# Optimization experiments

Measured on AMD Instinct MI355X. Metric: run time of the kernel, lower is better.

## Reference

```python
import jax, jax.numpy as jnp
import numpy as np

NPTS = 16
IN_FEATURES = 3


def setup_inputs() -> dict:
    key = jax.random.key(0)
    x = jax.random.uniform(key, (8, IN_FEATURES, 512, 512), dtype=jnp.float32)
    # parameters, matching the torch module's initialization
    shifts = np.linspace(0, 1, NPTS, endpoint=False, dtype=np.float32)[:, None]
    shift = jnp.asarray(np.tile(shifts, (1, IN_FEATURES)))          # (npts, C)
    slopes = np.zeros((NPTS, IN_FEATURES), dtype=np.float32)
    slopes[0, :] = 1.0
    slopes = jnp.asarray(slopes)                                    # (npts, C)
    conv_w = jnp.full((IN_FEATURES,), 1.0 / IN_FEATURES, dtype=jnp.float32)  # 1x1 conv C->1
    conv_b = jnp.zeros((1,), dtype=jnp.float32)
    return {"x": x, "shift": shift, "slopes": slopes, "conv_w": conv_w, "conv_b": conv_b}


def reference(x, shift, slopes, conv_w, conv_b):
    # x: (B, C, H, W); shift/slopes: (npts, C)
    # piecewise-linear curve: sum_p slopes[p,c] * relu(x - shift[p,c])
    curves = slopes[None, :, :, None, None] * jax.nn.relu(
        x[:, None, :, :, :] - shift[None, :, :, None, None]
    )                                   # (B, npts, C, H, W)
    y = jnp.sum(curves, axis=1)         # (B, C, H, W)
    # 1x1 conv C -> 1 with bias, then hardtanh(0, 1)
    out = jnp.einsum("bchw,c->bhw", y, conv_w)[:, None, :, :] + conv_b[None, :, None, None]
    return jnp.clip(out, 0.0, 1.0)      # (B, 1, H, W)
```

## Files before the change

kernel.cpp:

```cpp
#include <hip/hip_runtime.h>
#include <hip/hip_bf16.h>


constexpr int NPTS = 16;
constexpr int C    = 3;
constexpr int HW   = 512 * 512;
constexpr int HW4  = HW / 4;

__global__ __launch_bounds__(256)
void curve_channel_kernel(const float4* __restrict__ x,
                          const float*  __restrict__ shift,
                          const float*  __restrict__ slopes,
                          const float*  __restrict__ conv_w,
                          const float*  __restrict__ conv_b,
                          float4*       __restrict__ out,
                          int n4)
{
    const int idx = blockIdx.x * 256 + threadIdx.x;
    if (idx >= n4) return;

    const int b   = idx >> 16;
    const int hw4 = idx & (HW4 - 1);

    const float4* xb = x + (size_t)b * (C * HW4) + hw4;

    const float bias = conv_b[0];
    float ax = bias, ay = bias, az = bias, aw = bias;

#pragma unroll
    for (int c = 0; c < C; ++c) {
        const float4 xv = xb[(size_t)c * HW4];
        const float  w  = conv_w[c];
        float yx = 0.f, yy = 0.f, yz = 0.f, yw = 0.f;
#pragma unroll
        for (int p = 0; p < NPTS; ++p) {
            const float s = shift[p * C + c];
            const float m = slopes[p * C + c];
            yx += m * fmaxf(xv.x - s, 0.f);
            yy += m * fmaxf(xv.y - s, 0.f);
            yz += m * fmaxf(xv.z - s, 0.f);
            yw += m * fmaxf(xv.w - s, 0.f);
        }
        ax += w * yx;
        ay += w * yy;
        az += w * yz;
        aw += w * yw;
    }

    float4 o;
    o.x = fminf(fmaxf(ax, 0.f), 1.f);
    o.y = fminf(fmaxf(ay, 0.f), 1.f);
    o.z = fminf(fmaxf(az, 0.f), 1.f);
    o.w = fminf(fmaxf(aw, 0.f), 1.f);
    out[idx] = o;
}

extern "C" void kernel_launch(void* const* d_in, const int* in_sizes, int n_in,
                              void* d_out, int out_size, void* d_ws, size_t ws_size,
                              hipStream_t stream)
{
    const float* x      = (const float*)d_in[0];
    const float* shift  = (const float*)d_in[1];
    const float* slopes = (const float*)d_in[2];
    const float* conv_w = (const float*)d_in[3];
    const float* conv_b = (const float*)d_in[4];
    float*       out    = (float*)d_out;

    const int n4     = out_size / 4;
    const int blocks = (n4 + 255) / 256;

    curve_channel_kernel<<<dim3(blocks), dim3(256), 0, stream>>>(
        (const float4*)x, shift, slopes, conv_w, conv_b, (float4*)out, n4);
}
```

Measured before the change: 82.10 us.

## Rewrite relu sum via abs identity, process two float4 per thread, nontemporal stores

Uses relu(x-s) = 0.5*((x-s)+|x-s|) to fold the linear part into per-channel constants A and B, so each breakpoint costs one sub, one abs-modifier and one FMA instead of a max, a multiply and an add. Each thread now handles two float4 groups, which halves the grid and amortizes the shift/slope parameter loads. Output is written with nontemporal stores. The kernel is largely memory bound (about 25 MB read, 8 MB written), so the ALU savings may matter little, and the extra registers could reduce occupancy.

```diff
diff --git a/kernel.cpp b/kernel.cpp
--- a/kernel.cpp
+++ b/kernel.cpp
@@ -1,58 +1,78 @@
 #include <hip/hip_runtime.h>
-#include <hip/hip_bf16.h>
 
+
+typedef float f4v __attribute__((ext_vector_type(4)));
 
 constexpr int NPTS = 16;
 constexpr int C    = 3;
-constexpr int HW   = 512 * 512;
-constexpr int HW4  = HW / 4;
+constexpr int HW4  = 65536;
 
 __global__ __launch_bounds__(256)
-void curve_channel_kernel(const float4* __restrict__ x,
-                          const float*  __restrict__ shift,
-                          const float*  __restrict__ slopes,
-                          const float*  __restrict__ conv_w,
-                          const float*  __restrict__ conv_b,
-                          float4*       __restrict__ out,
+void curve_channel_kernel(const f4v*  __restrict__ x,
+                          const float* __restrict__ shift,
+                          const float* __restrict__ slopes,
+                          const float* __restrict__ conv_w,
+                          const float* __restrict__ conv_b,
+                          f4v*        __restrict__ out,
                           int n4)
 {
-    const int idx = blockIdx.x * 256 + threadIdx.x;
-    if (idx >= n4) return;
+    const int i0 = blockIdx.x * 512 + (int)threadIdx.x;
+    if (i0 >= n4) return;
+    const int  i1   = i0 + 256;
+    const bool has1 = (i1 < n4);
 
-    const int b   = idx >> 16;
-    const int hw4 = idx & (HW4 - 1);
-
-    const float4* xb = x + (size_t)b * (C * HW4) + hw4;
+    const int b0 = i0 >> 16, h0 = i0 & (HW4 - 1);
+    const int b1 = i1 >> 16, h1 = i1 & (HW4 - 1);
+    const f4v* xp0 = x + (size_t)b0 * (C * HW4) + h0;
+    const f4v* xp1 = x + (size_t)b1 * (C * HW4) + h1;
 
     const float bias = conv_b[0];
-    float ax = bias, ay = bias, az = bias, aw = bias;
+    float acc[8];
+#pragma unroll
+    for (int e = 0; e < 8; ++e) acc[e] = bias;
 
 #pragma unroll
     for (int c = 0; c < C; ++c) {
-        const float4 xv = xb[(size_t)c * HW4];
-        const float  w  = conv_w[c];
-        float yx = 0.f, yy = 0.f, yz = 0.f, yw = 0.f;
+        const f4v v0 = xp0[(size_t)c * HW4];
+        f4v v1 = (f4v){0.f, 0.f, 0.f, 0.f};
+        if (has1) v1 = xp1[(size_t)c * HW4];
+        const float xv[8] = { v0[0], v0[1], v0[2], v0[3],
+                              v1[0], v1[1], v1[2], v1[3] };
+        const float w = conv_w[c];
+
+        float sv[NPTS], hm[NPTS];
+        float A = 0.f, B = 0.f;
 #pragma unroll
         for (int p = 0; p < NPTS; ++p) {
-            const float s = shift[p * C + c];
-            const float m = slopes[p * C + c];
-            yx += m * fmaxf(xv.x - s, 0.f);
-            yy += m * fmaxf(xv.y - s, 0.f);
-            yz += m * fmaxf(xv.z - s, 0.f);
-            yw += m * fmaxf(xv.w - s, 0.f);
+            sv[p] = shift[p * C + c];
+            hm[p] = 0.5f * slopes[p * C + c];
+            A += hm[p];
+            B  = fmaf(-hm[p], sv[p], B);
         }
-        ax += w * yx;
-        ay += w * yy;
-        az += w * yz;
-        aw += w * yw;
+
+        float y[8];
+#pragma unroll
+        for (int e = 0; e < 8; ++e) y[e] = fmaf(A, xv[e], B);
+
+#pragma unroll
+        for (int p = 0; p < NPTS; ++p) {
+#pragma unroll
+            for (int e = 0; e < 8; ++e)
+                y[e] = fmaf(hm[p], fabsf(xv[e] - sv[p]), y[e]);
+        }
+
+#pragma unroll
+        for (int e = 0; e < 8; ++e) acc[e] = fmaf(w, y[e], acc[e]);
     }
 
-    float4 o;
-    o.x = fminf(fmaxf(ax, 0.f), 1.f);
-    o.y = fminf(fmaxf(ay, 0.f), 1.f);
-    o.z = fminf(fmaxf(az, 0.f), 1.f);
-    o.w = fminf(fmaxf(aw, 0.f), 1.f);
-    out[idx] = o;
+    f4v o0, o1;
+#pragma unroll
+    for (int e = 0; e < 4; ++e) o0[e] = fminf(fmaxf(acc[e],     0.f), 1.f);
+#pragma unroll
+    for (int e = 0; e < 4; ++e) o1[e] = fminf(fmaxf(acc[4 + e], 0.f), 1.f);
+
+    __builtin_nontemporal_store(o0, &out[i0]);
+    if (has1) __builtin_nontemporal_store(o1, &out[i1]);
 }
 
 extern "C" void kernel_launch(void* const* d_in, const int* in_sizes, int n_in,
@@ -64,11 +84,10 @@
     const float* slopes = (const float*)d_in[2];
     const float* conv_w = (const float*)d_in[3];
     const float* conv_b = (const float*)d_in[4];
-    float*       out    = (float*)d_out;
 
     const int n4     = out_size / 4;
-    const int blocks = (n4 + 255) / 256;
+    const int blocks = (n4 + 511) / 512;
 
     curve_channel_kernel<<<dim3(blocks), dim3(256), 0, stream>>>(
-        (const float4*)x, shift, slopes, conv_w, conv_b, (float4*)out, n4);
+        (const f4v*)x, shift, slopes, conv_w, conv_b, (f4v*)d_out, n4);
 }
```

Result: faster. 80.35 us (-2.1%).
